# Optimization experiments

Measured on AMD Instinct MI355X. Metric: run time of the kernel, lower is better.

Reference implementation:

```python
import jax, jax.numpy as jnp
import numpy as np

D_IN, D_CELL, T = 1024, 2048, 2048


def setup_inputs() -> dict:
    key = jax.random.key(0)
    ks = jax.random.split(key, 9)
    s = 1.0 / np.sqrt(D_IN + D_CELL)  # ~PyTorch Linear init scale
    def W(k):
        return jax.random.normal(k, (D_CELL, D_IN + D_CELL), dtype=jnp.float32) * s
    def b(k):
        return jax.random.normal(k, (D_CELL,), dtype=jnp.float32) * s
    return {
        "x": jax.random.normal(ks[0], (D_IN, T), dtype=jnp.float32),
        "W_forget": W(ks[1]), "b_forget": b(ks[2]),
        "W_input_sig": W(ks[3]), "b_input_sig": b(ks[4]),
        "W_input_tanh": W(ks[5]), "b_input_tanh": b(ks[6]),
        "W_output": W(ks[7]), "b_output": b(ks[8]),
    }


def reference(x, W_forget, b_forget, W_input_sig, b_input_sig,
              W_input_tanh, b_input_tanh, W_output, b_output):
    # x: [D_in, T]; weights: [D_cell, D_in+D_cell]; returns h: [D_cell, T]
    d_cell = W_forget.shape[0]
    # Fuse the 4 gate GEMVs into one [4*D_cell, D_in+D_cell] matmul per step.
    W_all = jnp.concatenate([W_forget, W_input_sig, W_input_tanh, W_output], axis=0)
    b_all = jnp.concatenate([b_forget, b_input_sig, b_input_tanh, b_output], axis=0)

    def step(carry, x_t):
        c, h = carry
        z = jnp.concatenate([x_t, h])               # [D_in + D_cell]
        g = W_all @ z + b_all                        # [4*D_cell]
        f = jax.nn.sigmoid(g[:d_cell])
        i = jax.nn.sigmoid(g[d_cell:2 * d_cell])
        cand = jnp.tanh(g[2 * d_cell:3 * d_cell])
        o = jax.nn.sigmoid(g[3 * d_cell:])
        c_new = f * c + i * cand
        h_new = o * jnp.tanh(c_new)
        return (c_new, h_new), h_new

    init = (jnp.zeros((d_cell,), x.dtype), jnp.zeros((d_cell,), x.dtype))
    _, hs = jax.lax.scan(step, init, x.T)            # hs: [T, D_cell]
    return hs.T                                      # [D_cell, T]
```

## Files before the change

kernel.cpp:

```cpp
#include <hip/hip_runtime.h>
#include <math.h>

#define D_IN    1024
#define D_CELL  2048
#define T_STEPS 2048
#define D_Z     3072
#define R_TOTAL (4 * D_CELL)
#define NBLK    256
#define NTHR    1024

typedef unsigned long long u64;

__global__ void lstm_init_kernel(u64* __restrict__ slots) {
    int i = blockIdx.x * 256 + threadIdx.x;
    if (i < 2 * D_CELL) slots[i] = 0ull;
}

__global__ __launch_bounds__(256) void lstm_gx_kernel(
    const float* __restrict__ Wf, const float* __restrict__ bf,
    const float* __restrict__ Wi, const float* __restrict__ bi,
    const float* __restrict__ Wc, const float* __restrict__ bc,
    const float* __restrict__ Wo, const float* __restrict__ bo,
    const float* __restrict__ x,  float* __restrict__ Gx)
{
    __shared__ float Wl[8][D_IN];
    const int tid = threadIdx.x;
    const int r0  = blockIdx.y * 8;
    const int g   = r0 >> 11;
    const int d0  = r0 & 2047;
    const float* W = (g == 0) ? Wf : (g == 1) ? Wi : (g == 2) ? Wc : Wo;
    const float* b = (g == 0) ? bf : (g == 1) ? bi : (g == 2) ? bc : bo;

    for (int idx = tid; idx < 8 * (D_IN / 4); idx += 256) {
        int jr = idx >> 8;
        int k4 = idx & 255;
        ((float4*)Wl[jr])[k4] =
            ((const float4*)(W + (size_t)(d0 + jr) * D_Z))[k4];
    }
    __syncthreads();

    const int t = blockIdx.x * 256 + tid;
    float acc[8];
#pragma unroll
    for (int jr = 0; jr < 8; ++jr) acc[jr] = 0.f;

    for (int k = 0; k < D_IN; k += 4) {
        float xv0 = x[(size_t)(k + 0) * T_STEPS + t];
        float xv1 = x[(size_t)(k + 1) * T_STEPS + t];
        float xv2 = x[(size_t)(k + 2) * T_STEPS + t];
        float xv3 = x[(size_t)(k + 3) * T_STEPS + t];
#pragma unroll
        for (int jr = 0; jr < 8; ++jr) {
            float4 w = ((const float4*)Wl[jr])[k >> 2];
            acc[jr] += w.x * xv0 + w.y * xv1 + w.z * xv2 + w.w * xv3;
        }
    }

#pragma unroll
    for (int jr = 0; jr < 8; ++jr) {
        int r = r0 + jr;
        Gx[(size_t)r * T_STEPS + t] = acc[jr] + b[d0 + jr];
    }
}

__global__ __launch_bounds__(NTHR, 4) void lstm_rec_kernel(
    const float* __restrict__ Wf, const float* __restrict__ Wi,
    const float* __restrict__ Wc, const float* __restrict__ Wo,
    const float* __restrict__ Gx, u64* __restrict__ slots,
    float* __restrict__ out)
{
    __shared__ float hs[D_CELL];
    __shared__ float gdot[32];
    __shared__ float cls[8];

    const int tid  = threadIdx.x;
    const int w    = tid >> 6;
    const int lane = tid & 63;
    const int r0   = 2 * w;

    const int g0 = r0 & 3,        g1 = (r0 + 1) & 3;
    const int cl = r0 >> 2;
    const int d  = blockIdx.x * 8 + cl;
    const float* Wb0 = ((g0 == 0) ? Wf : (g0 == 1) ? Wi : (g0 == 2) ? Wc : Wo)
                       + (size_t)d * D_Z + D_IN;
    const float* Wb1 = ((g1 == 0) ? Wf : (g1 == 1) ? Wi : (g1 == 2) ? Wc : Wo)
                       + (size_t)d * D_Z + D_IN;
    float4 wA[8], wB[8];
#pragma unroll
    for (int j = 0; j < 8; ++j) {
        wA[j] = *(const float4*)(Wb0 + j * 256 + lane * 4);
        wB[j] = *(const float4*)(Wb1 + j * 256 + lane * 4);
    }

    const int myrow = r0 + (lane & 1);
    const size_t gxbase = (size_t)((myrow & 3) * D_CELL
                                   + blockIdx.x * 8 + (myrow >> 2)) * T_STEPS;

    if (tid < 8) cls[tid] = 0.f;

    for (int t = 0; t < T_STEPS; ++t) {
        float gx_pref = 0.f;
        if (lane < 2) gx_pref = Gx[gxbase + t];

        if (t == 0) {
            hs[2 * tid]     = 0.f;
            hs[2 * tid + 1] = 0.f;
        } else {
            const u64* buf = slots + (size_t)(t & 1) * D_CELL;
            u64 a, b;
            while ((unsigned)((a = __hip_atomic_load(&buf[2 * tid],
                        __ATOMIC_RELAXED, __HIP_MEMORY_SCOPE_AGENT)) >> 32)
                   != (unsigned)t)
                __builtin_amdgcn_s_sleep(1);
            while ((unsigned)((b = __hip_atomic_load(&buf[2 * tid + 1],
                        __ATOMIC_RELAXED, __HIP_MEMORY_SCOPE_AGENT)) >> 32)
                   != (unsigned)t)
                __builtin_amdgcn_s_sleep(1);
            hs[2 * tid]     = __uint_as_float((unsigned)a);
            hs[2 * tid + 1] = __uint_as_float((unsigned)b);
        }
        __syncthreads();

        float acc0 = 0.f, acc1 = 0.f;
#pragma unroll
        for (int j = 0; j < 8; ++j) {
            float4 h = *(const float4*)(hs + j * 256 + lane * 4);
            acc0 += wA[j].x * h.x + wA[j].y * h.y + wA[j].z * h.z + wA[j].w * h.w;
            acc1 += wB[j].x * h.x + wB[j].y * h.y + wB[j].z * h.z + wB[j].w * h.w;
        }
        float vK = (lane & 1) ? acc1 : acc0;
        float vO = (lane & 1) ? acc0 : acc1;
        float v  = vK + __shfl_xor(vO, 1);
        v += __shfl_xor(v, 2);
        v += __shfl_xor(v, 4);
        v += __shfl_xor(v, 8);
        v += __shfl_xor(v, 16);
        v += __shfl_xor(v, 32);
        if (lane < 2) gdot[r0 + lane] = v + gx_pref;
        __syncthreads();

        if (tid < 8) {
            float gf = gdot[tid * 4 + 0], gi = gdot[tid * 4 + 1];
            float gc = gdot[tid * 4 + 2], go = gdot[tid * 4 + 3];
            float f    = 1.f / (1.f + expf(-gf));
            float ig   = 1.f / (1.f + expf(-gi));
            float cand = tanhf(gc);
            float o    = 1.f / (1.f + expf(-go));
            float cn   = f * cls[tid] + ig * cand;
            cls[tid] = cn;
            float hn = o * tanhf(cn);
            out[(size_t)(blockIdx.x * 8 + tid) * T_STEPS + t] = hn;
            if (t + 1 < T_STEPS) {
                u64 pk = ((u64)(unsigned)(t + 1) << 32)
                       | (u64)__float_as_uint(hn);
                __hip_atomic_store(
                    slots + (size_t)((t + 1) & 1) * D_CELL + blockIdx.x * 8 + tid,
                    pk, __ATOMIC_RELAXED, __HIP_MEMORY_SCOPE_AGENT);
            }
        }
    }
}

extern "C" void kernel_launch(void* const* d_in, const int* in_sizes, int n_in,
                              void* d_out, int out_size, void* d_ws, size_t ws_size,
                              hipStream_t stream) {
    const float* x  = (const float*)d_in[0];
    const float* Wf = (const float*)d_in[1];
    const float* bf = (const float*)d_in[2];
    const float* Wi = (const float*)d_in[3];
    const float* bi = (const float*)d_in[4];
    const float* Wc = (const float*)d_in[5];
    const float* bc = (const float*)d_in[6];
    const float* Wo = (const float*)d_in[7];
    const float* bo = (const float*)d_in[8];
    float* out = (float*)d_out;

    const size_t gx_elems = (size_t)R_TOTAL * T_STEPS;
    const size_t need = gx_elems * 4 + 2 * D_CELL * 8;
    if (ws_size < need) return;
    float* Gx    = (float*)d_ws;
    u64*   slots = (u64*)(Gx + gx_elems);

    lstm_init_kernel<<<16, 256, 0, stream>>>(slots);

    dim3 ggrid(T_STEPS / 256, R_TOTAL / 8);
    lstm_gx_kernel<<<ggrid, 256, 0, stream>>>(Wf, bf, Wi, bi, Wc, bc, Wo, bo,
                                              x, Gx);

    lstm_rec_kernel<<<NBLK, NTHR, 0, stream>>>(Wf, Wi, Wc, Wo, Gx, slots, out);
}
```

Baseline: 6.997 ms.

## Restructure recurrent LSTM kernel to one cell per wave with double-buffered h

The recurrent kernel now uses 512 threads per block with each wave owning one cell's four gates. The gate nonlinearities are computed in-register, which removes the second __syncthreads and the gdot/cls shared-memory round trip. The h buffer is double-buffered in LDS, and each thread polls four slots per iteration with a combined tag check. The input-projection kernel is also rewritten: it reads weights straight from global memory, computes four timesteps per thread, and remaps blocks across XCDs. Fast exp2/rcp intrinsics replace expf/tanhf, which may slightly change numerics.

```diff
diff --git a/kernel.cpp b/kernel.cpp
--- a/kernel.cpp
+++ b/kernel.cpp
@@ -7,7 +7,7 @@
 #define D_Z     3072
 #define R_TOTAL (4 * D_CELL)
 #define NBLK    256
-#define NTHR    1024
+#define NTHR    512
 
 typedef unsigned long long u64;
 
@@ -23,140 +23,169 @@
     const float* __restrict__ Wo, const float* __restrict__ bo,
     const float* __restrict__ x,  float* __restrict__ Gx)
 {
-    __shared__ float Wl[8][D_IN];
+    const int bid = blockIdx.x;
+    const int xcd = bid & 7;
+    const int loc = bid >> 3;
+    const int tx  = xcd >> 2;
+    const int yb  = (xcd & 3) * 256 + loc;
     const int tid = threadIdx.x;
-    const int r0  = blockIdx.y * 8;
+    const int t0  = tx * 1024 + tid * 4;
+    const int r0  = yb * 8;
     const int g   = r0 >> 11;
     const int d0  = r0 & 2047;
     const float* W = (g == 0) ? Wf : (g == 1) ? Wi : (g == 2) ? Wc : Wo;
     const float* b = (g == 0) ? bf : (g == 1) ? bi : (g == 2) ? bc : bo;
 
-    for (int idx = tid; idx < 8 * (D_IN / 4); idx += 256) {
-        int jr = idx >> 8;
-        int k4 = idx & 255;
-        ((float4*)Wl[jr])[k4] =
-            ((const float4*)(W + (size_t)(d0 + jr) * D_Z))[k4];
-    }
-    __syncthreads();
-
-    const int t = blockIdx.x * 256 + tid;
-    float acc[8];
-#pragma unroll
-    for (int jr = 0; jr < 8; ++jr) acc[jr] = 0.f;
+    const float* wr0 = W + (size_t)(d0 + 0) * D_Z;
+    const float* wr1 = W + (size_t)(d0 + 1) * D_Z;
+    const float* wr2 = W + (size_t)(d0 + 2) * D_Z;
+    const float* wr3 = W + (size_t)(d0 + 3) * D_Z;
+    const float* wr4 = W + (size_t)(d0 + 4) * D_Z;
+    const float* wr5 = W + (size_t)(d0 + 5) * D_Z;
+    const float* wr6 = W + (size_t)(d0 + 6) * D_Z;
+    const float* wr7 = W + (size_t)(d0 + 7) * D_Z;
+
+    float4 acc[8];
+#pragma unroll
+    for (int jr = 0; jr < 8; ++jr) acc[jr] = make_float4(0.f, 0.f, 0.f, 0.f);
 
     for (int k = 0; k < D_IN; k += 4) {
-        float xv0 = x[(size_t)(k + 0) * T_STEPS + t];
-        float xv1 = x[(size_t)(k + 1) * T_STEPS + t];
-        float xv2 = x[(size_t)(k + 2) * T_STEPS + t];
-        float xv3 = x[(size_t)(k + 3) * T_STEPS + t];
+        float4 xa = *(const float4*)(x + (size_t)(k + 0) * T_STEPS + t0);
+        float4 xb = *(const float4*)(x + (size_t)(k + 1) * T_STEPS + t0);
+        float4 xc = *(const float4*)(x + (size_t)(k + 2) * T_STEPS + t0);
+        float4 xd = *(const float4*)(x + (size_t)(k + 3) * T_STEPS + t0);
+        const float* wrs[8] = {wr0, wr1, wr2, wr3, wr4, wr5, wr6, wr7};
 #pragma unroll
         for (int jr = 0; jr < 8; ++jr) {
-            float4 w = ((const float4*)Wl[jr])[k >> 2];
-            acc[jr] += w.x * xv0 + w.y * xv1 + w.z * xv2 + w.w * xv3;
+            float4 w = *(const float4*)(wrs[jr] + k);
+            acc[jr].x += w.x * xa.x + w.y * xb.x + w.z * xc.x + w.w * xd.x;
+            acc[jr].y += w.x * xa.y + w.y * xb.y + w.z * xc.y + w.w * xd.y;
+            acc[jr].z += w.x * xa.z + w.y * xb.z + w.z * xc.z + w.w * xd.z;
+            acc[jr].w += w.x * xa.w + w.y * xb.w + w.z * xc.w + w.w * xd.w;
         }
     }
 
 #pragma unroll
     for (int jr = 0; jr < 8; ++jr) {
-        int r = r0 + jr;
-        Gx[(size_t)r * T_STEPS + t] = acc[jr] + b[d0 + jr];
-    }
-}
-
-__global__ __launch_bounds__(NTHR, 4) void lstm_rec_kernel(
+        float bb = b[d0 + jr];
+        float4 o = acc[jr];
+        o.x += bb; o.y += bb; o.z += bb; o.w += bb;
+        *(float4*)(Gx + (size_t)(r0 + jr) * T_STEPS + t0) = o;
+    }
+}
+
+__global__ __launch_bounds__(NTHR, 2) void lstm_rec_kernel(
     const float* __restrict__ Wf, const float* __restrict__ Wi,
     const float* __restrict__ Wc, const float* __restrict__ Wo,
     const float* __restrict__ Gx, u64* __restrict__ slots,
     float* __restrict__ out)
 {
-    __shared__ float hs[D_CELL];
-    __shared__ float gdot[32];
-    __shared__ float cls[8];
+    __shared__ float hs[2][D_CELL];
 
     const int tid  = threadIdx.x;
     const int w    = tid >> 6;
     const int lane = tid & 63;
-    const int r0   = 2 * w;
-
-    const int g0 = r0 & 3,        g1 = (r0 + 1) & 3;
-    const int cl = r0 >> 2;
-    const int d  = blockIdx.x * 8 + cl;
-    const float* Wb0 = ((g0 == 0) ? Wf : (g0 == 1) ? Wi : (g0 == 2) ? Wc : Wo)
-                       + (size_t)d * D_Z + D_IN;
-    const float* Wb1 = ((g1 == 0) ? Wf : (g1 == 1) ? Wi : (g1 == 2) ? Wc : Wo)
-                       + (size_t)d * D_Z + D_IN;
-    float4 wA[8], wB[8];
+    const int d    = blockIdx.x * 8 + w;
+
+    const float* bse0 = Wf + (size_t)d * D_Z + D_IN;
+    const float* bse1 = Wi + (size_t)d * D_Z + D_IN;
+    const float* bse2 = Wc + (size_t)d * D_Z + D_IN;
+    const float* bse3 = Wo + (size_t)d * D_Z + D_IN;
+    float4 wg0[8], wg1[8], wg2[8], wg3[8];
 #pragma unroll
     for (int j = 0; j < 8; ++j) {
-        wA[j] = *(const float4*)(Wb0 + j * 256 + lane * 4);
-        wB[j] = *(const float4*)(Wb1 + j * 256 + lane * 4);
-    }
-
-    const int myrow = r0 + (lane & 1);
-    const size_t gxbase = (size_t)((myrow & 3) * D_CELL
-                                   + blockIdx.x * 8 + (myrow >> 2)) * T_STEPS;
-
-    if (tid < 8) cls[tid] = 0.f;
+        wg0[j] = *(const float4*)(bse0 + j * 256 + lane * 4);
+        wg1[j] = *(const float4*)(bse1 + j * 256 + lane * 4);
+        wg2[j] = *(const float4*)(bse2 + j * 256 + lane * 4);
+        wg3[j] = *(const float4*)(bse3 + j * 256 + lane * 4);
+    }
+
+    const size_t gxbase = (size_t)((lane & 3) * D_CELL + d) * T_STEPS;
+
+    const int sidx = w * 256 + lane * 4;
+
+    float c = 0.f;
 
     for (int t = 0; t < T_STEPS; ++t) {
-        float gx_pref = 0.f;
-        if (lane < 2) gx_pref = Gx[gxbase + t];
-
+        float gx = 0.f;
+        if (lane < 4) gx = Gx[gxbase + t];
+
+        const int par = t & 1;
         if (t == 0) {
-            hs[2 * tid]     = 0.f;
-            hs[2 * tid + 1] = 0.f;
+            *(float4*)&hs[0][sidx] = make_float4(0.f, 0.f, 0.f, 0.f);
         } else {
-            const u64* buf = slots + (size_t)(t & 1) * D_CELL;
-            u64 a, b;
-            while ((unsigned)((a = __hip_atomic_load(&buf[2 * tid],
-                        __ATOMIC_RELAXED, __HIP_MEMORY_SCOPE_AGENT)) >> 32)
-                   != (unsigned)t)
+            const u64* bp = slots + (size_t)par * D_CELL + sidx;
+            const u64 tg = (u64)(unsigned)t << 32;
+            u64 s0, s1, s2, s3;
+            for (;;) {
+                s0 = __hip_atomic_load(bp + 0, __ATOMIC_RELAXED, __HIP_MEMORY_SCOPE_AGENT);
+                s1 = __hip_atomic_load(bp + 1, __ATOMIC_RELAXED, __HIP_MEMORY_SCOPE_AGENT);
+                s2 = __hip_atomic_load(bp + 2, __ATOMIC_RELAXED, __HIP_MEMORY_SCOPE_AGENT);
+                s3 = __hip_atomic_load(bp + 3, __ATOMIC_RELAXED, __HIP_MEMORY_SCOPE_AGENT);
+                u64 m = ((s0 ^ tg) | (s1 ^ tg) | (s2 ^ tg) | (s3 ^ tg)) >> 32;
+                if (m == 0) break;
                 __builtin_amdgcn_s_sleep(1);
-            while ((unsigned)((b = __hip_atomic_load(&buf[2 * tid + 1],
-                        __ATOMIC_RELAXED, __HIP_MEMORY_SCOPE_AGENT)) >> 32)
-                   != (unsigned)t)
-                __builtin_amdgcn_s_sleep(1);
-            hs[2 * tid]     = __uint_as_float((unsigned)a);
-            hs[2 * tid + 1] = __uint_as_float((unsigned)b);
+            }
+            float4 hv;
+            hv.x = __uint_as_float((unsigned)s0);
+            hv.y = __uint_as_float((unsigned)s1);
+            hv.z = __uint_as_float((unsigned)s2);
+            hv.w = __uint_as_float((unsigned)s3);
+            *(float4*)&hs[par][sidx] = hv;
         }
         __syncthreads();
 
-        float acc0 = 0.f, acc1 = 0.f;
+        float a0 = 0.f, a1 = 0.f, a2 = 0.f, a3 = 0.f;
 #pragma unroll
         for (int j = 0; j < 8; ++j) {
-            float4 h = *(const float4*)(hs + j * 256 + lane * 4);
-            acc0 += wA[j].x * h.x + wA[j].y * h.y + wA[j].z * h.z + wA[j].w * h.w;
-            acc1 += wB[j].x * h.x + wB[j].y * h.y + wB[j].z * h.z + wB[j].w * h.w;
-        }
-        float vK = (lane & 1) ? acc1 : acc0;
-        float vO = (lane & 1) ? acc0 : acc1;
-        float v  = vK + __shfl_xor(vO, 1);
-        v += __shfl_xor(v, 2);
-        v += __shfl_xor(v, 4);
-        v += __shfl_xor(v, 8);
-        v += __shfl_xor(v, 16);
-        v += __shfl_xor(v, 32);
-        if (lane < 2) gdot[r0 + lane] = v + gx_pref;
-        __syncthreads();
-
-        if (tid < 8) {
-            float gf = gdot[tid * 4 + 0], gi = gdot[tid * 4 + 1];
-            float gc = gdot[tid * 4 + 2], go = gdot[tid * 4 + 3];
-            float f    = 1.f / (1.f + expf(-gf));
-            float ig   = 1.f / (1.f + expf(-gi));
-            float cand = tanhf(gc);
-            float o    = 1.f / (1.f + expf(-go));
-            float cn   = f * cls[tid] + ig * cand;
-            cls[tid] = cn;
-            float hn = o * tanhf(cn);
-            out[(size_t)(blockIdx.x * 8 + tid) * T_STEPS + t] = hn;
+            float4 h = *(const float4*)&hs[par][j * 256 + lane * 4];
+            a0 += wg0[j].x * h.x + wg0[j].y * h.y + wg0[j].z * h.z + wg0[j].w * h.w;
+            a1 += wg1[j].x * h.x + wg1[j].y * h.y + wg1[j].z * h.z + wg1[j].w * h.w;
+            a2 += wg2[j].x * h.x + wg2[j].y * h.y + wg2[j].z * h.z + wg2[j].w * h.w;
+            a3 += wg3[j].x * h.x + wg3[j].y * h.y + wg3[j].z * h.z + wg3[j].w * h.w;
+        }
+
+        float p01a = (lane & 1) ? a1 : a0;
+        float p01b = (lane & 1) ? a0 : a1;
+        float v01  = p01a + __shfl_xor(p01b, 1);
+        float p23a = (lane & 1) ? a3 : a2;
+        float p23b = (lane & 1) ? a2 : a3;
+        float v23  = p23a + __shfl_xor(p23b, 1);
+        float qa = (lane & 2) ? v23 : v01;
+        float qb = (lane & 2) ? v01 : v23;
+        float u  = qa + __shfl_xor(qb, 2);
+        u += __shfl_xor(u, 4);
+        u += __shfl_xor(u, 8);
+        u += __shfl_xor(u, 16);
+        u += __shfl_xor(u, 32);
+        u += gx;
+
+        float gf = __shfl(u, 0);
+        float gi = __shfl(u, 1);
+        float gc = __shfl(u, 2);
+        float go = __shfl(u, 3);
+
+        const float L2E  = 1.442695041f;
+        const float L2E2 = 2.885390082f;
+        float f  = __builtin_amdgcn_rcpf(1.f + __builtin_amdgcn_exp2f(-L2E * gf));
+        float ig = __builtin_amdgcn_rcpf(1.f + __builtin_amdgcn_exp2f(-L2E * gi));
+        float o  = __builtin_amdgcn_rcpf(1.f + __builtin_amdgcn_exp2f(-L2E * go));
+        float ec = __builtin_amdgcn_exp2f(L2E2 * gc);
+        float cand = 1.f - 2.f * __builtin_amdgcn_rcpf(ec + 1.f);
+        c = f * c + ig * cand;
+        float eh = __builtin_amdgcn_exp2f(L2E2 * c);
+        float tc = 1.f - 2.f * __builtin_amdgcn_rcpf(eh + 1.f);
+        float hn = o * tc;
+
+        if (lane == 0) {
             if (t + 1 < T_STEPS) {
                 u64 pk = ((u64)(unsigned)(t + 1) << 32)
                        | (u64)__float_as_uint(hn);
                 __hip_atomic_store(
-                    slots + (size_t)((t + 1) & 1) * D_CELL + blockIdx.x * 8 + tid,
+                    slots + (size_t)((t + 1) & 1) * D_CELL + d,
                     pk, __ATOMIC_RELAXED, __HIP_MEMORY_SCOPE_AGENT);
             }
+            out[(size_t)d * T_STEPS + t] = hn;
         }
     }
 }
@@ -183,9 +212,8 @@
 
     lstm_init_kernel<<<16, 256, 0, stream>>>(slots);
 
-    dim3 ggrid(T_STEPS / 256, R_TOTAL / 8);
-    lstm_gx_kernel<<<ggrid, 256, 0, stream>>>(Wf, bf, Wi, bi, Wc, bc, Wo, bo,
-                                              x, Gx);
+    lstm_gx_kernel<<<2048, 256, 0, stream>>>(Wf, bf, Wi, bi, Wc, bc, Wo, bo,
+                                             x, Gx);
 
     lstm_rec_kernel<<<NBLK, NTHR, 0, stream>>>(Wf, Wi, Wc, Wo, Gx, slots, out);
 }
```

New measurement: 13.33 ms. +90.5%, slower.
